# Performance work log

Hardware: AMD Instinct MI355X
Metric: run time of the kernel (lower is better)

Reference implementation:

```python
import jax, jax.numpy as jnp
import numpy as np

IN_CH = 1024   # backbone channels
N_T = 81       # n_targets (COCO classes + bg)
K = 7          # PSROI grid size
H = 100        # feature map height
WID = 100      # feature map width
R = 1024       # number of regions
S = 2          # bilinear sampling points per bin edge (PSROIAlign-style average)


def setup_inputs() -> dict:
    key = jax.random.key(0)
    k1, k2, k3 = jax.random.split(key, 3)
    x = jax.random.normal(k1, (IN_CH, H, WID), dtype=jnp.float32)
    # regions: fractional (i, j, h, w) = (center_y, center_x, height, width) in [0,1]
    regions = jax.random.uniform(k2, (R, 4), dtype=jnp.float32)
    conv_w = jax.random.normal(k3, (N_T * K * K, IN_CH), dtype=jnp.float32) * 0.02
    conv_b = jnp.zeros((N_T * K * K,), dtype=jnp.float32)
    return {"x": x, "regions": regions, "conv_w": conv_w, "conv_b": conv_b}


def _bilinear_pool(map_thw, ys, xs):
    """Average of bilinear samples of one bin's score map.

    map_thw: (T, H, W) score map for this (u, v) bin's channel group.
    ys: (R, S) sample row coords.  xs: (R, S) sample col coords.
    Returns (R, T): per-region average-pooled bin value.
    """
    Hm, Wm = map_thw.shape[1], map_thw.shape[2]
    ys = jnp.clip(ys, 0.0, Hm - 1)
    xs = jnp.clip(xs, 0.0, Wm - 1)
    y0 = jnp.floor(ys)
    x0 = jnp.floor(xs)
    y0i = y0.astype(jnp.int32)
    x0i = x0.astype(jnp.int32)
    y1i = jnp.minimum(y0i + 1, Hm - 1)
    x1i = jnp.minimum(x0i + 1, Wm - 1)
    wy1 = ys - y0
    wy0 = 1.0 - wy1
    wx1 = xs - x0
    wx0 = 1.0 - wx1

    def g(yi, xi):  # gather (T, R, S, S)
        return map_thw[:, yi[:, :, None], xi[:, None, :]]

    v = (g(y0i, x0i) * (wy0[:, :, None] * wx0[:, None, :])
         + g(y0i, x1i) * (wy0[:, :, None] * wx1[:, None, :])
         + g(y1i, x0i) * (wy1[:, :, None] * wx0[:, None, :])
         + g(y1i, x1i) * (wy1[:, :, None] * wx1[:, None, :]))
    return v.mean((2, 3)).T  # (R, T)


def reference(x, regions, conv_w, conv_b):
    # 1x1 conv score map: (n_targets*k^2, H, W)
    sm = jnp.einsum('oc,chw->ohw', conv_w, x) + conv_b[:, None, None]
    sm = sm.reshape(N_T, K, K, H, WID)  # (T, ky, kx, H, W) position-sensitive groups

    # region geometry (fractional center/size -> absolute feature-map coords)
    top = (regions[:, 0] - regions[:, 2] * 0.5) * H     # (R,)
    left = (regions[:, 1] - regions[:, 3] * 0.5) * WID  # (R,)
    bh = regions[:, 2] * H / K                          # bin height
    bw = regions[:, 3] * WID / K                        # bin width

    off = (jnp.arange(S, dtype=jnp.float32) + 0.5) / S  # (S,) sample offsets in bin
    bins = jnp.arange(K, dtype=jnp.float32)             # (K,)
    ys = top[:, None, None] + (bins[None, :, None] + off[None, None, :]) * bh[:, None, None]   # (R,K,S)
    xs = left[:, None, None] + (bins[None, :, None] + off[None, None, :]) * bw[:, None, None]  # (R,K,S)

    # vmap over the k x k position-sensitive bins; bin (u,v) reads channel group (:,u,v)
    inner = jax.vmap(_bilinear_pool, in_axes=(1, None, 1))  # over kx: sm axis, xs axis
    outer = jax.vmap(inner, in_axes=(1, 1, None))           # over ky: sm axis, ys axis
    pooled = outer(sm, ys, xs)  # (K, K, R, T)

    # pooled.mean(-1).mean(-1) over the k x k grid
    scores = pooled.mean((0, 1))  # (R, T)
    return scores
```

## Files before the change

kernel.cpp:

```cpp
#include <hip/hip_runtime.h>
#include <cstddef>

#define IN_CH 1024
#define NT    81
#define KGRID 7
#define NBINS 49
#define HH    100
#define WW    100
#define NPIX  (HH*WW)
#define NREG  1024
#define COLB  82
#define NCOL  (NBINS*COLB)
#define NPADW 4096
#define SBIN  84
#define SROWB (NBINS*SBIN)
#define NG    8
#define NSC   2560
#define PXB   ((NPIX + 31) / 32)
#define PXG   (PXB * (IN_CH / 128))
#define PREPG (PXG + NPADW)

#define GM_T  40
#define GN_T  16
#define NKT   16

typedef unsigned short ushortT;
typedef short bf16x8 __attribute__((ext_vector_type(8)));
typedef float f32x4  __attribute__((ext_vector_type(4)));

static __device__ __forceinline__ unsigned short f2bf(float f) {
    unsigned int u = __builtin_bit_cast(unsigned int, f);
    return (unsigned short)((u + 0x7fffu + ((u >> 16) & 1u)) >> 16);
}

static __device__ __forceinline__ void gld_lds16(const ushortT* g, ushortT* l) {
    __builtin_amdgcn_global_load_lds(
        (__attribute__((address_space(1))) void*)(unsigned long long)(uintptr_t)g,
        (__attribute__((address_space(3))) void*)(unsigned int)(unsigned long long)(uintptr_t)l,
        16, 0, 0);
}

static __device__ __forceinline__ void barf() {
    asm volatile("" ::: "memory");
    __builtin_amdgcn_s_barrier();
    asm volatile("" ::: "memory");
}

__global__ __launch_bounds__(256) void prep_fused(const float* __restrict__ x,
                                                  ushortT* __restrict__ xbT,
                                                  const float* __restrict__ conv_w,
                                                  ushortT* __restrict__ Wr) {
    __shared__ float tile[128][33];
    const int tid = threadIdx.x;
    const int bid = blockIdx.x;
    if (bid < PXG) {
        const int p0 = (bid % PXB) * 32;
        const int c0 = (bid / PXB) * 128;
        const int pl = tid & 31;
        const int cg = tid >> 5;
        const int p = p0 + pl;
#pragma unroll
        for (int it = 0; it < 16; ++it) {
            const int c = it * 8 + cg;
            tile[c][pl] = (p < NPIX) ? x[(size_t)(c0 + c) * NPIX + p] : 0.0f;
        }
        __syncthreads();
#pragma unroll
        for (int pass = 0; pass < 2; ++pass) {
            const int pix = pass * 16 + (tid >> 4);
            const int cb  = (tid & 15) * 8;
            if (p0 + pix < NPIX) {
                uint4 pk;
                pk.x = (unsigned int)f2bf(tile[cb + 0][pix]) | ((unsigned int)f2bf(tile[cb + 1][pix]) << 16);
                pk.y = (unsigned int)f2bf(tile[cb + 2][pix]) | ((unsigned int)f2bf(tile[cb + 3][pix]) << 16);
                pk.z = (unsigned int)f2bf(tile[cb + 4][pix]) | ((unsigned int)f2bf(tile[cb + 5][pix]) << 16);
                pk.w = (unsigned int)f2bf(tile[cb + 6][pix]) | ((unsigned int)f2bf(tile[cb + 7][pix]) << 16);
                *(uint4*)(xbT + (size_t)(p0 + pix) * IN_CH + c0 + cb) = pk;
            }
        }
    } else {
        const int row = bid - PXG;
        const int bin = row / COLB;
        const int t   = row - bin * COLB;
        const int c   = tid * 4;
        uint2 pk; pk.x = 0; pk.y = 0;
        if (bin < NBINS && t < NT) {
            const float4 v = *(const float4*)(conv_w + ((size_t)(t * NBINS + bin)) * IN_CH + c);
            pk.x = (unsigned int)f2bf(v.x) | ((unsigned int)f2bf(v.y) << 16);
            pk.y = (unsigned int)f2bf(v.z) | ((unsigned int)f2bf(v.w) << 16);
        }
        *(uint2*)(Wr + (size_t)row * IN_CH + c) = pk;
    }
}

__global__ __launch_bounds__(512, 2) void gemm_sm(const ushortT* __restrict__ xbT,
                                                  const ushortT* __restrict__ Wr,
                                                  unsigned char* __restrict__ sm,
                                                  float* __restrict__ scales) {
    __shared__ ushortT lA[2][16384];
    __shared__ ushortT lB[2][16384];

    const int tid  = threadIdx.x;
    const int lane = tid & 63;
    const int w    = tid >> 6;
    const int wm   = w & 1;
    const int wn   = w >> 1;

    const int bid   = blockIdx.x;
    const int sw    = (bid & 7) * 80 + (bid >> 3);
    const int mtile = sw >> 4;
    const int ntile = sw & 15;
    const int p0 = mtile * 256;
    const int n0 = ntile * 256;

    const int l3   = lane >> 3;
    const int srco = ((lane & 7) ^ l3) << 3;
    const int w2   = w * 2;

    const ushortT* gA[2][2];
    const ushortT* gB[2][2];
    int dstA[2][2];
#pragma unroll
    for (int h = 0; h < 2; ++h)
#pragma unroll
        for (int it = 0; it < 2; ++it) {
            const int hr = (w2 + it) * 8 + l3;
            int p = p0 + h * 128 + hr; if (p > NPIX - 1) p = NPIX - 1;
            gA[h][it] = xbT + (size_t)p * IN_CH + srco;
            gB[h][it] = Wr + (size_t)(n0 + h * 128 + hr) * IN_CH + srco;
            dstA[h][it] = h * 8192 + (w2 + it) * 512 + lane * 8;
        }

#define STAGE_A(bb, h, T) { gld_lds16(gA[h][0] + (size_t)(T) * 64, &lA[bb][dstA[h][0]]); \
                            gld_lds16(gA[h][1] + (size_t)(T) * 64, &lA[bb][dstA[h][1]]); }
#define STAGE_B(bb, h, T) { gld_lds16(gB[h][0] + (size_t)(T) * 64, &lB[bb][dstA[h][0]]); \
                            gld_lds16(gB[h][1] + (size_t)(T) * 64, &lB[bb][dstA[h][1]]); }

    const int m_l = lane & 15;
    const int kq  = lane >> 4;
    const int ph0 = ((kq) ^ (lane & 7)) << 3;
    const int ph1 = ((4 + kq) ^ (lane & 7)) << 3;
    const int arow = (wm * 128 + m_l) * 64;
    const int brow = (wn * 64 + m_l) * 64;

#define RD_A(bb, mq) { _Pragma("unroll") for (int mt = 0; mt < 4; ++mt) { \
        const int ro = arow + ((mq) * 64 + mt * 16) * 64; \
        af[mt][0] = *(const bf16x8*)(&lA[bb][ro + ph0]); \
        af[mt][1] = *(const bf16x8*)(&lA[bb][ro + ph1]); } }
#define RD_B(dst, bb, nq) { _Pragma("unroll") for (int nt = 0; nt < 2; ++nt) { \
        const int ro = brow + ((nq) * 32 + nt * 16) * 64; \
        dst[nt][0] = *(const bf16x8*)(&lB[bb][ro + ph0]); \
        dst[nt][1] = *(const bf16x8*)(&lB[bb][ro + ph1]); } }
#define MM(mq, B, nq) { _Pragma("unroll") for (int mt = 0; mt < 4; ++mt) \
        _Pragma("unroll") for (int nt = 0; nt < 2; ++nt) { \
        acc[mq][mt][nq][nt] = __builtin_amdgcn_mfma_f32_16x16x32_bf16(af[mt][0], B[nt][0], acc[mq][mt][nq][nt], 0, 0, 0); \
        acc[mq][mt][nq][nt] = __builtin_amdgcn_mfma_f32_16x16x32_bf16(af[mt][1], B[nt][1], acc[mq][mt][nq][nt], 0, 0, 0); } }

    f32x4 acc[2][4][2][2];
#pragma unroll
    for (int a = 0; a < 2; ++a)
#pragma unroll
        for (int b = 0; b < 4; ++b)
#pragma unroll
            for (int c = 0; c < 2; ++c)
#pragma unroll
                for (int d = 0; d < 2; ++d) acc[a][b][c][d] = (f32x4){0.f, 0.f, 0.f, 0.f};

    bf16x8 af[4][2], bf0[2][2], bf1[2][2];

    STAGE_A(0, 0, 0); STAGE_A(0, 1, 0); STAGE_B(0, 0, 0); STAGE_B(0, 1, 0);
    STAGE_A(1, 0, 1); STAGE_A(1, 1, 1); STAGE_B(1, 0, 1); STAGE_B(1, 1, 1);
    asm volatile("s_waitcnt vmcnt(8)" ::: "memory");
    __builtin_amdgcn_s_barrier();
    asm volatile("" ::: "memory");

#pragma unroll 2
    for (int kt = 0; kt < NKT; ++kt) {
        const int b = kt & 1;
        RD_A(b, 0);
        RD_B(bf0, b, 0);
        barf();
        __builtin_amdgcn_s_setprio(1);
        MM(0, bf0, 0);
        __builtin_amdgcn_s_setprio(0);
        barf();
        RD_B(bf1, b, 1);
        barf();
        __builtin_amdgcn_s_setprio(1);
        MM(0, bf1, 1);
        __builtin_amdgcn_s_setprio(0);
        barf();
        RD_A(b, 1);
        if (kt < NKT - 2) { STAGE_B(b, 0, kt + 2); STAGE_B(b, 1, kt + 2); }
        barf();
        __builtin_amdgcn_s_setprio(1);
        MM(1, bf1, 1);
        __builtin_amdgcn_s_setprio(0);
        barf();
        __builtin_amdgcn_s_setprio(1);
        MM(1, bf0, 0);
        __builtin_amdgcn_s_setprio(0);
        if (kt < NKT - 2) {
            STAGE_A(b, 0, kt + 2); STAGE_A(b, 1, kt + 2);
            asm volatile("s_waitcnt vmcnt(8)" ::: "memory");
        } else {
            asm volatile("s_waitcnt vmcnt(0)" ::: "memory");
        }
        __builtin_amdgcn_s_barrier();
        asm volatile("" ::: "memory");
    }

    __syncthreads();
    float am = 0.0f;
#pragma unroll
    for (int mq = 0; mq < 2; ++mq)
#pragma unroll
        for (int mt = 0; mt < 4; ++mt)
#pragma unroll
            for (int nq = 0; nq < 2; ++nq)
#pragma unroll
                for (int nt = 0; nt < 2; ++nt)
#pragma unroll
                    for (int rg = 0; rg < 4; ++rg)
                        am = fmaxf(am, fabsf(acc[mq][mt][nq][nt][rg]));
#pragma unroll
    for (int off = 32; off > 0; off >>= 1) am = fmaxf(am, __shfl_xor(am, off));
    float* red = (float*)lA;
    if (lane == 0) red[w] = am;
    __syncthreads();
    const float qam = fmaxf(fmaxf(red[w], red[w ^ 2]), 1e-30f);
    const float inv = 127.0f / qam;
    if (lane == 0 && (wn & 1) == 0)
        scales[(mtile * 2 + wm) * 32 + ntile * 2 + (wn >> 1)] = qam * (1.0f / 127.0f);

    const int prow0 = p0 + wm * 128 + kq * 4;
    const int ncol0 = n0 + wn * 64 + m_l;
    int  coloff[2][2];
    bool cok[2][2];
#pragma unroll
    for (int nq = 0; nq < 2; ++nq)
#pragma unroll
        for (int nt = 0; nt < 2; ++nt) {
            const int n = ncol0 + nq * 32 + nt * 16;
            cok[nq][nt] = (n < NCOL);
            coloff[nq][nt] = n + 2 * (n / COLB);
        }
#pragma unroll
    for (int mq = 0; mq < 2; ++mq)
#pragma unroll
        for (int mt = 0; mt < 4; ++mt)
#pragma unroll
            for (int rg = 0; rg < 4; ++rg) {
                const int p = prow0 + mq * 64 + mt * 16 + rg;
                if (p < NPIX) {
                    unsigned char* rowp = sm + (size_t)p * SROWB;
#pragma unroll
                    for (int nq = 0; nq < 2; ++nq)
#pragma unroll
                        for (int nt = 0; nt < 2; ++nt)
                            if (cok[nq][nt]) {
                                const int q = __float2int_rn(acc[mq][mt][nq][nt][rg] * inv);
                                rowp[coloff[nq][nt]] = (unsigned char)(signed char)q;
                            }
                }
            }
#undef STAGE_A
#undef STAGE_B
#undef RD_A
#undef RD_B
#undef MM
}

__global__ __launch_bounds__(256) void pool_kernel(const unsigned char* __restrict__ sm,
                                                   const float* __restrict__ scales,
                                                   const float* __restrict__ regions,
                                                   const float* __restrict__ conv_b,
                                                   float* __restrict__ out) {
    __shared__ int   rowo[28]; __shared__ float roww[28];
    __shared__ int   coli[28]; __shared__ float colw[28];
    __shared__ int   pofs[120];
    __shared__ float pw[120];
    __shared__ int   pptb[120];
    __shared__ int   pnb[120];
    __shared__ float part[40][100];
    const int tid = threadIdx.x;
    const int r = blockIdx.x;
    const int g = blockIdx.y;

    if (tid < 28) {
        const float4 reg = *(const float4*)(regions + (size_t)r * 4);
        const float top = (reg.x - reg.z * 0.5f) * (float)HH;
        const float bh  = reg.z * ((float)HH / (float)KGRID);
        const int u = tid >> 2, i = tid & 3;
        const int s = i >> 1, hi = i & 1;
        float y = top + ((float)u + ((float)s + 0.5f) * 0.5f) * bh;
        y = fminf(fmaxf(y, 0.0f), (float)(HH - 1));
        const float y0f = floorf(y);
        const int y0 = (int)y0f;
        const float wy1 = y - y0f;
        rowo[tid] = (hi ? min(y0 + 1, HH - 1) : y0) * WW;
        roww[tid] = hi ? wy1 : (1.0f - wy1);
    } else if (tid >= 32 && tid < 60) {
        const float4 reg = *(const float4*)(regions + (size_t)r * 4);
        const float left = (reg.y - reg.w * 0.5f) * (float)WW;
        const float bw   = reg.w * ((float)WW / (float)KGRID);
        const int idx = tid - 32;
        const int v = idx >> 2, j = idx & 3;
        const int s = j >> 1, hi = j & 1;
        float xx = left + ((float)v + ((float)s + 0.5f) * 0.5f) * bw;
        xx = fminf(fmaxf(xx, 0.0f), (float)(WW - 1));
        const float x0f = floorf(xx);
        const int x0 = (int)x0f;
        const float wx1 = xx - x0f;
        coli[idx] = hi ? min(x0 + 1, WW - 1) : x0;
        colw[idx] = hi ? wx1 : (1.0f - wx1);
    }
    __syncthreads();
    if (tid < 120) {
        if (tid < 98) {
            const int tt = g * 98 + tid;
            const int bin = tt >> 4, tap = tt & 15;
            const int u = bin / KGRID, v = bin - u * KGRID;
            const int i = tap >> 2, j = tap & 3;
            const int pix = rowo[u * 4 + i] + coli[v * 4 + j];
            pofs[tid] = pix * SROWB + bin * SBIN;
            pw[tid]   = roww[u * 4 + i] * colw[v * 4 + j] * (1.0f / 196.0f);
            pptb[tid] = (pix >> 7) * 32;
            pnb[tid]  = bin * COLB;
        } else {
            pofs[tid] = 0;
            pw[tid]   = 0.0f;
            pptb[tid] = 0;
            pnb[tid]  = 0;
        }
    }
    __syncthreads();

    const int lane = tid & 63, w = tid >> 6;
    const int sub  = lane / 6;
    const int cg   = lane - sub * 6;
    if (sub < 10) {
        const int str = w * 10 + sub;
        uint4 v[3];
#pragma unroll
        for (int it = 0; it < 3; ++it)
            v[it] = *(const uint4*)(sm + pofs[it * 40 + str] + cg * 16);

        float acc[16];
#pragma unroll
        for (int ch = 0; ch < 16; ++ch) acc[ch] = 0.0f;
#pragma unroll
        for (int it = 0; it < 3; ++it) {
            const int l  = it * 40 + str;
            const float wt = pw[l];
            const int nb  = pnb[l] + cg * 16;
            const int nt0 = nb >> 7;
            const int rr  = nb & 127;
            const float s0 = scales[pptb[l] + nt0];
            const float s1 = scales[pptb[l] + nt0 + 1];
            const float w0 = wt * s0, w1 = wt * s1;
            const unsigned int uu[4] = {v[it].x, v[it].y, v[it].z, v[it].w};
#pragma unroll
            for (int b = 0; b < 4; ++b) {
#pragma unroll
                for (int k = 0; k < 4; ++k) {
                    const int ch = b * 4 + k;
                    const int q = (int)(signed char)((uu[b] >> (k * 8)) & 0xff);
                    acc[ch] += ((rr < 128 - ch) ? w0 : w1) * (float)q;
                }
            }
        }
#pragma unroll
        for (int b = 0; b < 4; ++b) {
            float4 p4;
            p4.x = acc[b * 4]; p4.y = acc[b * 4 + 1];
            p4.z = acc[b * 4 + 2]; p4.w = acc[b * 4 + 3];
            *(float4*)&part[str][cg * 16 + b * 4] = p4;
        }
    }
    __syncthreads();
    if (tid < NT) {
        float vv = 0.f;
#pragma unroll
        for (int s = 0; s < 40; ++s) vv += part[s][tid];
        if (g == 0) {
            float bsum = 0.f;
            for (int bin = 0; bin < NBINS; ++bin) bsum += conv_b[tid * NBINS + bin];
            vv += bsum * (1.0f / (float)NBINS);
        }
        atomicAdd(out + (size_t)r * NT + tid, vv);
    }
}

__global__ __launch_bounds__(256) void xpose_kernel(const float* __restrict__ x,
                                                    float* __restrict__ xt) {
    __shared__ float tile[32][33];
    const int p0 = blockIdx.x * 32;
    const int c0 = blockIdx.y * 32;
    const int tx = threadIdx.x;
    const int ty = threadIdx.y;
#pragma unroll
    for (int k = 0; k < 32; k += 8) {
        const int p = p0 + tx;
        if (p < NPIX) tile[ty + k][tx] = x[(size_t)(c0 + ty + k) * NPIX + p];
    }
    __syncthreads();
#pragma unroll
    for (int k = 0; k < 32; k += 8) {
        const int p = p0 + ty + k;
        if (p < NPIX) xt[(size_t)p * IN_CH + (c0 + tx)] = tile[tx][ty + k];
    }
}

template <bool XPOSED>
__global__ __launch_bounds__(256) void psroi_kernel(
    const float* __restrict__ xsrc, const float* __restrict__ regions,
    const float* __restrict__ conv_w, const float* __restrict__ conv_b,
    float* __restrict__ out) {
    __shared__ float w_lds[32 * 96];
    __shared__ float g_lds[32 * 64];
    __shared__ int   rowoff[64][4];
    __shared__ float rowwf[64][4];
    __shared__ int   colidx[64][4];
    __shared__ float colwf[64][4];
    const int tid = threadIdx.x;
    const int bin = blockIdx.x >> 4;
    const int rg  = blockIdx.x & 15;
    const int u = bin / KGRID, v = bin % KGRID;
    const int r0 = rg * 64;
    if (tid < 64) {
        const float4 reg = *(const float4*)(regions + (size_t)(r0 + tid) * 4);
        const float top  = (reg.x - reg.z * 0.5f) * (float)HH;
        const float left = (reg.y - reg.w * 0.5f) * (float)WW;
        const float bh = reg.z * ((float)HH / (float)KGRID);
        const float bw = reg.w * ((float)WW / (float)KGRID);
        const float scale = 1.0f / 196.0f;
#pragma unroll
        for (int s = 0; s < 2; s++) {
            const float off = (s + 0.5f) * 0.5f;
            float yy = top + ((float)u + off) * bh;
            yy = fminf(fmaxf(yy, 0.0f), (float)(HH - 1));
            const float y0f = floorf(yy);
            const int y0 = (int)y0f;
            const float wy1 = yy - y0f;
            rowoff[tid][2 * s] = y0 * WW;
            rowoff[tid][2 * s + 1] = min(y0 + 1, HH - 1) * WW;
            rowwf[tid][2 * s] = (1.0f - wy1) * scale;
            rowwf[tid][2 * s + 1] = wy1 * scale;
            float xx = left + ((float)v + off) * bw;
            xx = fminf(fmaxf(xx, 0.0f), (float)(WW - 1));
            const float x0f = floorf(xx);
            const int x0 = (int)x0f;
            const float wx1 = xx - x0f;
            colidx[tid][2 * s] = x0;
            colidx[tid][2 * s + 1] = min(x0 + 1, WW - 1);
            colwf[tid][2 * s] = 1.0f - wx1;
            colwf[tid][2 * s + 1] = wx1;
        }
    }
    const int ri = tid & 15, tq = tid >> 4, rb = tid >> 2, cq = tid & 3;
    float acc[4][6];
#pragma unroll
    for (int m = 0; m < 4; m++)
#pragma unroll
        for (int k = 0; k < 6; k++) acc[m][k] = 0.0f;
    for (int chunk = 0; chunk < IN_CH / 32; chunk++) {
        const int c0 = chunk * 32;
        __syncthreads();
#pragma unroll
        for (int it = 0; it < 12; it++) {
            const int idx = it * 256 + tid;
            const int t = idx >> 5, c = idx & 31;
            float val = 0.0f;
            if (t < NT) val = conv_w[(size_t)(t * NBINS + bin) * IN_CH + c0 + c];
            w_lds[c * 96 + t] = val;
        }
        const int cbase = c0 + cq * 8;
        float g8[8];
#pragma unroll
        for (int cc = 0; cc < 8; cc++) g8[cc] = 0.0f;
#pragma unroll
        for (int i = 0; i < 4; i++) {
            const int ro = rowoff[rb][i];
            const float wy = rowwf[rb][i];
#pragma unroll
            for (int j = 0; j < 4; j++) {
                const int pix = ro + colidx[rb][j];
                const float wv = wy * colwf[rb][j];
                if (XPOSED) {
                    const float4* p = (const float4*)(xsrc + (size_t)pix * IN_CH + cbase);
                    const float4 a = p[0]; const float4 b = p[1];
                    g8[0] += wv * a.x; g8[1] += wv * a.y; g8[2] += wv * a.z; g8[3] += wv * a.w;
                    g8[4] += wv * b.x; g8[5] += wv * b.y; g8[6] += wv * b.z; g8[7] += wv * b.w;
                } else {
#pragma unroll
                    for (int cc = 0; cc < 8; cc++)
                        g8[cc] += wv * xsrc[(size_t)(cbase + cc) * NPIX + pix];
                }
            }
        }
#pragma unroll
        for (int cc = 0; cc < 8; cc++) g_lds[(cq * 8 + cc) * 64 + rb] = g8[cc];
        __syncthreads();
#pragma unroll 4
        for (int c = 0; c < 32; c++) {
            float wv[6];
#pragma unroll
            for (int k = 0; k < 6; k++) wv[k] = w_lds[c * 96 + tq * 6 + k];
            const float4 gq = *(const float4*)&g_lds[c * 64 + ri * 4];
            const float gm[4] = {gq.x, gq.y, gq.z, gq.w};
#pragma unroll
            for (int m = 0; m < 4; m++)
#pragma unroll
                for (int k = 0; k < 6; k++) acc[m][k] += gm[m] * wv[k];
        }
    }
    const float invK2 = 1.0f / 49.0f;
#pragma unroll
    for (int k = 0; k < 6; k++) {
        const int t = tq * 6 + k;
        if (t < NT) {
            const float bterm = conv_b[t * NBINS + bin] * invK2;
#pragma unroll
            for (int m = 0; m < 4; m++) {
                const int rr = r0 + ri * 4 + m;
                atomicAdd(&out[(size_t)rr * NT + t], acc[m][k] + bterm);
            }
        }
    }
}

extern "C" void kernel_launch(void* const* d_in, const int* in_sizes, int n_in,
                              void* d_out, int out_size, void* d_ws, size_t ws_size,
                              hipStream_t stream) {
    const float* x       = (const float*)d_in[0];
    const float* regions = (const float*)d_in[1];
    const float* conv_w  = (const float*)d_in[2];
    const float* conv_b  = (const float*)d_in[3];
    float* out = (float*)d_out;

    const size_t sz_xbT = (size_t)NPIX * IN_CH * 2;
    const size_t sz_Wr  = (size_t)NPADW * IN_CH * 2;
    const size_t sz_sm  = (size_t)NPIX * SROWB + 256;
    const size_t sz_sc  = (size_t)NSC * sizeof(float);
    const size_t need   = sz_xbT + sz_Wr + sz_sm + sz_sc;

    if (ws_size >= need) {
        ushortT* xbT = (ushortT*)d_ws;
        ushortT* Wr  = (ushortT*)((char*)d_ws + sz_xbT);
        unsigned char* sm = (unsigned char*)d_ws + sz_xbT + sz_Wr;
        float* scales = (float*)((char*)d_ws + sz_xbT + sz_Wr + sz_sm);
        hipMemsetAsync(out, 0, (size_t)out_size * sizeof(float), stream);
        prep_fused<<<dim3(PREPG), 256, 0, stream>>>(x, xbT, conv_w, Wr);
        gemm_sm<<<dim3(GM_T * GN_T), 512, 0, stream>>>(xbT, Wr, sm, scales);
        pool_kernel<<<dim3(NREG, NG), 256, 0, stream>>>(sm, scales, regions, conv_b, out);
    } else {
        hipMemsetAsync(out, 0, (size_t)out_size * sizeof(float), stream);
        const size_t xt_bytes = (size_t)NPIX * IN_CH * sizeof(float);
        const dim3 mainGrid(NBINS * 16);
        if (ws_size >= xt_bytes) {
            float* xt = (float*)d_ws;
            xpose_kernel<<<dim3((NPIX + 31) / 32, IN_CH / 32), dim3(32, 8), 0, stream>>>(x, xt);
            psroi_kernel<true><<<mainGrid, 256, 0, stream>>>(xt, regions, conv_w, conv_b, out);
        } else {
            psroi_kernel<false><<<mainGrid, 256, 0, stream>>>(x, regions, conv_w, conv_b, out);
        }
    }
}
```

Measured before the change: 226.5 us.

## Interleave GEMM global-to-LDS staging row-by-row across MFMA phases

Restructures the staging of the bf16 GEMM (1x1 conv) K-loop. Global-to-LDS loads are now issued per 64-row slice and spread between the MFMA phases, instead of in two bursts. The loop is manually unrolled by two buffers, and one of the end-of-iteration barriers is replaced with a mid-iteration vmcnt wait. The aim is to overlap memory traffic with matrix math more evenly and to cut stall bubbles. This adds a risk of LDS read/write hazards, because staging now writes into the buffer still being read within the same iteration, so it relies on the exact barrier and wait placement.

New measurement: 221.7 us. 1.02x faster.

```diff
diff --git a/kernel.cpp b/kernel.cpp
--- a/kernel.cpp
+++ b/kernel.cpp
@@ -113,28 +113,20 @@
     const int p0 = mtile * 256;
     const int n0 = ntile * 256;
 
-    const int l3   = lane >> 3;
-    const int srco = ((lane & 7) ^ l3) << 3;
-    const int w2   = w * 2;
-
-    const ushortT* gA[2][2];
-    const ushortT* gB[2][2];
-    int dstA[2][2];
-#pragma unroll
-    for (int h = 0; h < 2; ++h)
-#pragma unroll
-        for (int it = 0; it < 2; ++it) {
-            const int hr = (w2 + it) * 8 + l3;
-            int p = p0 + h * 128 + hr; if (p > NPIX - 1) p = NPIX - 1;
-            gA[h][it] = xbT + (size_t)p * IN_CH + srco;
-            gB[h][it] = Wr + (size_t)(n0 + h * 128 + hr) * IN_CH + srco;
-            dstA[h][it] = h * 8192 + (w2 + it) * 512 + lane * 8;
-        }
-
-#define STAGE_A(bb, h, T) { gld_lds16(gA[h][0] + (size_t)(T) * 64, &lA[bb][dstA[h][0]]); \
-                            gld_lds16(gA[h][1] + (size_t)(T) * 64, &lA[bb][dstA[h][1]]); }
-#define STAGE_B(bb, h, T) { gld_lds16(gB[h][0] + (size_t)(T) * 64, &lB[bb][dstA[h][0]]); \
-                            gld_lds16(gB[h][1] + (size_t)(T) * 64, &lB[bb][dstA[h][1]]); }
+    const int srow = w * 8 + (lane >> 3);
+    const int srco = ((lane & 7) ^ (lane >> 3)) << 3;
+    const ushortT* gAr[4];
+    const ushortT* gBr[4];
+    int dstR[4];
+#pragma unroll
+    for (int r = 0; r < 4; ++r) {
+        int p = p0 + r * 64 + srow; if (p > NPIX - 1) p = NPIX - 1;
+        gAr[r] = xbT + (size_t)p * IN_CH + srco;
+        gBr[r] = Wr + (size_t)(n0 + r * 64 + srow) * IN_CH + srco;
+        dstR[r] = r * 4096 + w * 512 + lane * 8;
+    }
+#define STG_A(bb, r, T) gld_lds16(gAr[r] + (size_t)(T) * 64, &lA[bb][dstR[r]])
+#define STG_B(bb, r, T) gld_lds16(gBr[r] + (size_t)(T) * 64, &lB[bb][dstR[r]])
 
     const int m_l = lane & 15;
     const int kq  = lane >> 4;
@@ -155,6 +147,7 @@
         _Pragma("unroll") for (int nt = 0; nt < 2; ++nt) { \
         acc[mq][mt][nq][nt] = __builtin_amdgcn_mfma_f32_16x16x32_bf16(af[mt][0], B[nt][0], acc[mq][mt][nq][nt], 0, 0, 0); \
         acc[mq][mt][nq][nt] = __builtin_amdgcn_mfma_f32_16x16x32_bf16(af[mt][1], B[nt][1], acc[mq][mt][nq][nt], 0, 0, 0); } }
+#define PMM(mq, B, nq) { __builtin_amdgcn_s_setprio(1); MM(mq, B, nq); __builtin_amdgcn_s_setprio(0); }
 
     f32x4 acc[2][4][2][2];
 #pragma unroll
@@ -168,46 +161,71 @@
 
     bf16x8 af[4][2], bf0[2][2], bf1[2][2];
 
-    STAGE_A(0, 0, 0); STAGE_A(0, 1, 0); STAGE_B(0, 0, 0); STAGE_B(0, 1, 0);
-    STAGE_A(1, 0, 1); STAGE_A(1, 1, 1); STAGE_B(1, 0, 1); STAGE_B(1, 1, 1);
+#pragma unroll
+    for (int r = 0; r < 4; ++r) STG_A(0, r, 0);
+#pragma unroll
+    for (int r = 0; r < 4; ++r) STG_B(0, r, 0);
+#pragma unroll
+    for (int r = 0; r < 4; ++r) STG_A(1, r, 1);
+#pragma unroll
+    for (int r = 0; r < 4; ++r) STG_B(1, r, 1);
     asm volatile("s_waitcnt vmcnt(8)" ::: "memory");
     __builtin_amdgcn_s_barrier();
     asm volatile("" ::: "memory");
 
-#pragma unroll 2
-    for (int kt = 0; kt < NKT; ++kt) {
-        const int b = kt & 1;
-        RD_A(b, 0);
-        RD_B(bf0, b, 0);
-        barf();
-        __builtin_amdgcn_s_setprio(1);
-        MM(0, bf0, 0);
-        __builtin_amdgcn_s_setprio(0);
-        barf();
-        RD_B(bf1, b, 1);
-        barf();
-        __builtin_amdgcn_s_setprio(1);
-        MM(0, bf1, 1);
-        __builtin_amdgcn_s_setprio(0);
-        barf();
-        RD_A(b, 1);
-        if (kt < NKT - 2) { STAGE_B(b, 0, kt + 2); STAGE_B(b, 1, kt + 2); }
-        barf();
-        __builtin_amdgcn_s_setprio(1);
-        MM(1, bf1, 1);
-        __builtin_amdgcn_s_setprio(0);
-        barf();
-        __builtin_amdgcn_s_setprio(1);
-        MM(1, bf0, 0);
-        __builtin_amdgcn_s_setprio(0);
-        if (kt < NKT - 2) {
-            STAGE_A(b, 0, kt + 2); STAGE_A(b, 1, kt + 2);
+#pragma unroll 1
+    for (int i = 0; i < NKT / 2; ++i) {
+        const bool st = (i < NKT / 2 - 1);
+        const int t2 = 2 * i + 2;
+        const int t3 = 2 * i + 3;
+        RD_A(0, 0); RD_B(bf0, 0, 0);
+        barf();
+        PMM(0, bf0, 0);
+        barf();
+        RD_B(bf1, 0, 1);
+        if (st) { STG_A(0, 0, t2); STG_A(0, 2, t2); }
+        barf();
+        PMM(0, bf1, 1);
+        barf();
+        RD_A(0, 1);
+        if (st) { STG_B(0, 0, t2); STG_B(0, 1, t2); }
+        barf();
+        PMM(1, bf1, 1);
+        barf();
+        if (st) {
+            STG_A(0, 1, t2); STG_A(0, 3, t2);
+            asm volatile("s_waitcnt vmcnt(6)" ::: "memory");
+        } else {
+            asm volatile("s_waitcnt vmcnt(0)" ::: "memory");
+        }
+        barf();
+        PMM(1, bf0, 0);
+        barf();
+        RD_A(1, 0); RD_B(bf0, 1, 0);
+        if (st) { STG_B(0, 2, t2); STG_B(0, 3, t2); }
+        barf();
+        PMM(0, bf0, 0);
+        barf();
+        RD_B(bf1, 1, 1);
+        if (st) { STG_A(1, 0, t3); STG_A(1, 2, t3); }
+        barf();
+        PMM(0, bf1, 1);
+        barf();
+        RD_A(1, 1);
+        if (st) { STG_B(1, 0, t3); STG_B(1, 1, t3); }
+        barf();
+        PMM(1, bf1, 1);
+        barf();
+        if (st) {
+            STG_A(1, 1, t3); STG_A(1, 3, t3);
+            STG_B(1, 2, t3); STG_B(1, 3, t3);
             asm volatile("s_waitcnt vmcnt(8)" ::: "memory");
         } else {
             asm volatile("s_waitcnt vmcnt(0)" ::: "memory");
         }
-        __builtin_amdgcn_s_barrier();
-        asm volatile("" ::: "memory");
+        barf();
+        PMM(1, bf0, 0);
+        barf();
     }
 
     __syncthreads();
@@ -264,11 +282,12 @@
                             }
                 }
             }
-#undef STAGE_A
-#undef STAGE_B
+#undef STG_A
+#undef STG_B
 #undef RD_A
 #undef RD_B
 #undef MM
+#undef PMM
 }
 
 __global__ __launch_bounds__(256) void pool_kernel(const unsigned char* __restrict__ sm,
```
